# Optimization experiments

Hardware: AMD Instinct MI355X
Metric: run time of the kernel (lower is better)

Reference implementation:

```python
import jax, jax.numpy as jnp
import numpy as np

N_HEADS = 8
HIDDEN = 256
D_HEAD = HIDDEN // N_HEADS
N_NODES = 4096
N_EDGES = 16384


def setup_inputs() -> dict:
    key = jax.random.key(0)
    ks = jax.random.split(key, 12)
    s = 0.05
    return {
        "q": jax.random.normal(ks[0], (N_EDGES, HIDDEN), jnp.float32),
        "k": jax.random.normal(ks[1], (N_NODES, HIDDEN), jnp.float32),
        "v": jax.random.normal(ks[2], (N_NODES, HIDDEN), jnp.float32),
        "T": jax.random.uniform(ks[3], (N_NODES, N_EDGES), jnp.float32),
        "Wq": jax.random.normal(ks[4], (HIDDEN, HIDDEN), jnp.float32) * s,
        "bq": jax.random.normal(ks[5], (HIDDEN,), jnp.float32) * s,
        "Wk": jax.random.normal(ks[6], (HIDDEN, HIDDEN), jnp.float32) * s,
        "bk": jax.random.normal(ks[7], (HIDDEN,), jnp.float32) * s,
        "Wv": jax.random.normal(ks[8], (HIDDEN, HIDDEN), jnp.float32) * s,
        "bv": jax.random.normal(ks[9], (HIDDEN,), jnp.float32) * s,
        "Wo": jax.random.normal(ks[10], (HIDDEN, HIDDEN), jnp.float32) * s,
        "bo": jax.random.normal(ks[11], (HIDDEN,), jnp.float32) * s,
    }


def reference(q, k, v, T, Wq, bq, Wk, bk, Wv, bv, Wo, bo):
    scale = D_HEAD ** (-0.5)
    # projections, reshaped to per-head layout
    qh = (q @ Wq.T + bq).reshape(-1, N_HEADS, D_HEAD)  # [E, H, d]
    kh = (k @ Wk.T + bk).reshape(-1, N_HEADS, D_HEAD)  # [N, H, d]
    vh = (v @ Wv.T + bv).reshape(-1, N_HEADS, D_HEAD)  # [N, H, d]
    # row-normalized transition matrix (rows with zero sum left unscaled)
    row_sum = jnp.sum(T, axis=-1, keepdims=True)       # [N, 1]
    Tn = T / jnp.where(row_sum == 0, 1.0, row_sum)     # [N, E]
    # edge->node aggregation of queries, then scale
    qn = jnp.einsum("ne,ehd->nhd", Tn, qh) * scale     # [N, H, d]
    # attention: full NxN scores per head
    scores = jnp.einsum("nhd,mhd->hnm", qn, kh)        # [H, N, N]
    attn = jax.nn.softmax(scores, axis=-1)
    ctx = jnp.einsum("hnm,mhd->nhd", attn, vh)         # [N, H, d]
    out = ctx.reshape(-1, N_HEADS * D_HEAD) @ Wo.T + bo  # [N, hidden]
    return out
```

## Files before the change

### kernel.cpp

```cpp
#include <hip/hip_runtime.h>


#define N_NODES 4096
#define N_EDGES 16384
#define HIDDEN  256
#define KSPLIT  16

typedef __attribute__((ext_vector_type(4))) float f32x4;
typedef __attribute__((ext_vector_type(8))) short s16x8;
typedef __attribute__((ext_vector_type(4))) unsigned short u16x4;
typedef __attribute__((ext_vector_type(8))) unsigned short u16x8;

__device__ __forceinline__ unsigned short f2bf(float f) {
    union { float f; unsigned u; } x; x.f = f;
    unsigned r = x.u + 0x7FFFu + ((x.u >> 16) & 1u);
    return (unsigned short)(r >> 16);
}
__device__ __forceinline__ s16x8 pack8s(f32x4 x, f32x4 y) {
    u16x8 o;
    o[0]=f2bf(x[0]); o[1]=f2bf(x[1]); o[2]=f2bf(x[2]); o[3]=f2bf(x[3]);
    o[4]=f2bf(y[0]); o[5]=f2bf(y[1]); o[6]=f2bf(y[2]); o[7]=f2bf(y[3]);
    union { u16x8 u; s16x8 s; } c; c.u = o; return c.s;
}

__global__ __launch_bounds__(256)
void cvtW(const float* __restrict__ Wq, const float* __restrict__ Wk,
          const float* __restrict__ Wv, const float* __restrict__ Wo,
          unsigned short* __restrict__ dst)
{
    const int g = blockIdx.x * 256 + threadIdx.x;
    const long base = (long)g * 8;
    const int mat = (int)(base >> 16), off = (int)(base & 65535);
    const float* src = (mat == 0) ? Wq : (mat == 1) ? Wk : (mat == 2) ? Wv : Wo;
    f32x4 x = *(const f32x4*)&src[off];
    f32x4 y = *(const f32x4*)&src[off + 4];
    union { u16x8 u; s16x8 s; } c; c.s = pack8s(x, y);
    *(u16x8*)&dst[base] = c.u;
}

template<int MODE>
__global__ __launch_bounds__(256)
void proj_mfma(const float* __restrict__ A, const unsigned short* __restrict__ Wbf,
               const float* __restrict__ bias, unsigned short* __restrict__ out, int M)
{
    const int t = threadIdx.x;
    const int w = t >> 6, l = t & 63, lo = l & 15, h4 = l >> 4;
    const int m0 = blockIdx.x * 64 + w * 16;
    const int bn = blockIdx.y * 64;
    const float* Ar = A + (long)(m0 + lo) * 256 + h4 * 8;

    f32x4 acc[4] = {};
    #pragma unroll
    for (int kk = 0; kk < 8; ++kk) {
        f32x4 x = *(const f32x4*)&Ar[kk * 32];
        f32x4 y = *(const f32x4*)&Ar[kk * 32 + 4];
        s16x8 af = pack8s(x, y);
        #pragma unroll
        for (int nj = 0; nj < 4; ++nj) {
            s16x8 bf = *(const s16x8*)&Wbf[(bn + nj * 16 + lo) * 256 + kk * 32 + h4 * 8];
            acc[nj] = __builtin_amdgcn_mfma_f32_16x16x32_bf16(af, bf, acc[nj], 0, 0, 0);
        }
    }
    #pragma unroll
    for (int nj = 0; nj < 4; ++nj) {
        const int n = bn + nj * 16 + lo;
        const float bi = bias[n];
        if (MODE == 1) {
            #pragma unroll
            for (int r = 0; r < 4; ++r)
                out[(long)(m0 + h4 * 4 + r) * 256 + n] = f2bf(acc[nj][r] + bi);
        } else {
            u16x4 o;
            #pragma unroll
            for (int r = 0; r < 4; ++r) o[r] = f2bf(acc[nj][r] + bi);
            *(u16x4*)&out[(long)n * M + m0 + h4 * 4] = o;
        }
    }
}

__global__ __launch_bounds__(256)
void proj_out_mfma(const float* __restrict__ pctx, const float* __restrict__ plp,
                   const unsigned short* __restrict__ Wobf, const float* __restrict__ bo,
                   float* __restrict__ out)
{
    const int t = threadIdx.x;
    const int w = t >> 6, l = t & 63, lo = l & 15, h4 = l >> 4;
    const int m0 = blockIdx.x * 64 + w * 16;
    const int bn = blockIdx.y * 64;
    const int m = m0 + lo;

    float inv[8];
    #pragma unroll
    for (int h = 0; h < 8; ++h) {
        float s = plp[(0 * 8 + h) * N_NODES + m] + plp[(1 * 8 + h) * N_NODES + m]
                + plp[(2 * 8 + h) * N_NODES + m] + plp[(3 * 8 + h) * N_NODES + m];
        inv[h] = 1.0f / s;
    }
    const float* P = pctx + (long)m * 256;
    const long PS = (long)N_NODES * 256;

    f32x4 acc[4] = {};
    #pragma unroll
    for (int kk = 0; kk < 8; ++kk) {
        const int off = kk * 32 + h4 * 8;
        f32x4 x = *(const f32x4*)&P[off]          + *(const f32x4*)&P[PS + off]
                + *(const f32x4*)&P[2 * PS + off] + *(const f32x4*)&P[3 * PS + off];
        f32x4 y = *(const f32x4*)&P[off + 4]          + *(const f32x4*)&P[PS + off + 4]
                + *(const f32x4*)&P[2 * PS + off + 4] + *(const f32x4*)&P[3 * PS + off + 4];
        s16x8 af = pack8s(x * inv[kk], y * inv[kk]);
        #pragma unroll
        for (int nj = 0; nj < 4; ++nj) {
            s16x8 bf = *(const s16x8*)&Wobf[(bn + nj * 16 + lo) * 256 + kk * 32 + h4 * 8];
            acc[nj] = __builtin_amdgcn_mfma_f32_16x16x32_bf16(af, bf, acc[nj], 0, 0, 0);
        }
    }
    #pragma unroll
    for (int nj = 0; nj < 4; ++nj) {
        const int n = bn + nj * 16 + lo;
        const float bi = bo[n];
        #pragma unroll
        for (int r = 0; r < 4; ++r)
            out[(long)(m0 + h4 * 4 + r) * 256 + n] = acc[nj][r] + bi;
    }
}

__global__ __launch_bounds__(512, 4)
void tgemm(const float* __restrict__ T, const unsigned short* __restrict__ Bt,
           float* __restrict__ part, float* __restrict__ rsp)
{
    __shared__ __align__(16) unsigned short Bsm[2][256 * 64];
    const int t  = threadIdx.x;
    const int ks = blockIdx.x & 15, ms = blockIdx.x >> 4;
    const int m0 = ms * 128;
    const long k00 = (long)ks * 1024;
    const int w = t >> 6, l = t & 63, lo = l & 15, h4 = l >> 4;

    const int kx = ((l & 7) * 8) ^ ((l >> 3) << 3);
    const unsigned short* Bsrc = Bt + k00 + kx;

#define STAGE(itv, bufv) do {                                                       \
    const unsigned short* _s = Bsrc + (long)(itv) * 64;                             \
    unsigned short* _d = &Bsm[(bufv)][w * 2048];                                    \
    _Pragma("unroll")                                                               \
    for (int _i = 0; _i < 4; ++_i)                                                  \
        __builtin_amdgcn_global_load_lds(                                           \
            (const __attribute__((address_space(1))) unsigned int*)                 \
                (_s + (long)(w * 32 + _i * 8 + (l >> 3)) * N_EDGES),                \
            (__attribute__((address_space(3))) unsigned int*)(_d + _i * 512),       \
            16, 0, 0);                                                              \
} while (0)

    const float* Arow = T + (long)(m0 + w * 16 + lo) * N_EDGES + k00 + h4 * 8;

    STAGE(0, 0);
    f32x4 a0 = *(const f32x4*)&Arow[0];
    f32x4 a1 = *(const f32x4*)&Arow[4];
    f32x4 a2 = *(const f32x4*)&Arow[32];
    f32x4 a3 = *(const f32x4*)&Arow[36];
    __syncthreads();

    f32x4 acc[16] = {};
    float rs = 0.f;

    for (int it = 0; it < 16; ++it) {
        const int cur = it & 1;
        if (it < 15) STAGE(it + 1, cur ^ 1);
        s16x8 af0 = pack8s(a0, a1);
        s16x8 af1 = pack8s(a2, a3);
        rs += a0[0]+a0[1]+a0[2]+a0[3] + a1[0]+a1[1]+a1[2]+a1[3]
            + a2[0]+a2[1]+a2[2]+a2[3] + a3[0]+a3[1]+a3[2]+a3[3];
        if (it < 15) {
            const float* An = Arow + (it + 1) * 64;
            a0 = *(const f32x4*)&An[0];
            a1 = *(const f32x4*)&An[4];
            a2 = *(const f32x4*)&An[32];
            a3 = *(const f32x4*)&An[36];
        }
        const unsigned short* Bb = Bsm[cur];
        const int swz = (lo & 7) << 3;
        #pragma unroll
        for (int nj = 0; nj < 16; ++nj) {
            const int jb = (nj * 16 + lo) * 64;
            s16x8 bf0 = *(const s16x8*)&Bb[jb + ((h4 * 8) ^ swz)];
            s16x8 bf1 = *(const s16x8*)&Bb[jb + ((32 + h4 * 8) ^ swz)];
            acc[nj] = __builtin_amdgcn_mfma_f32_16x16x32_bf16(af0, bf0, acc[nj], 0, 0, 0);
            acc[nj] = __builtin_amdgcn_mfma_f32_16x16x32_bf16(af1, bf1, acc[nj], 0, 0, 0);
        }
        __syncthreads();
    }
#undef STAGE

    rs += __shfl_xor(rs, 16); rs += __shfl_xor(rs, 32);
    if (h4 == 0) rsp[ks * N_NODES + m0 + w * 16 + lo] = rs;

    float* P = part + (long)ks * (N_NODES * HIDDEN);
    #pragma unroll
    for (int nj = 0; nj < 16; ++nj)
        #pragma unroll
        for (int r = 0; r < 4; ++r)
            P[(long)(m0 + w * 16 + h4 * 4 + r) * HIDDEN + nj * 16 + lo] = acc[nj][r];
}

__global__ __launch_bounds__(256)
void finalize(const float* __restrict__ part, const float* __restrict__ rsp,
              unsigned short* __restrict__ qn)
{
    const int idx = blockIdx.x * 256 + threadIdx.x;
    const long i4 = (long)idx * 4;
    const int n = (int)(i4 >> 8);
    f32x4 s = {};
    #pragma unroll
    for (int ksp = 0; ksp < KSPLIT; ++ksp)
        s += *(const f32x4*)&part[(long)ksp * (N_NODES * HIDDEN) + i4];
    float rs = 0.f;
    #pragma unroll
    for (int ksp = 0; ksp < KSPLIT; ++ksp) rs += rsp[ksp * N_NODES + n];
    rs = (rs == 0.0f) ? 1.0f : rs;
    const float sc = 0.17677669529663687f / rs;
    u16x4 o;
    #pragma unroll
    for (int i = 0; i < 4; ++i) o[i] = f2bf(s[i] * sc);
    *(u16x4*)&qn[i4] = o;
}

__global__ __launch_bounds__(256)
void attn(const unsigned short* __restrict__ qn, const unsigned short* __restrict__ kh,
          const unsigned short* __restrict__ vht, float* __restrict__ pctx,
          float* __restrict__ plp)
{
    __shared__ __align__(16) unsigned short Ksm[64 * 40];
    __shared__ __align__(16) unsigned short Vsm[32 * 72];
    __shared__ __align__(16) unsigned short Psm[4][32 * 72];
    const int t  = threadIdx.x;
    const int hh = blockIdx.x >> 7, nb = (blockIdx.x >> 2) & 31, mh = blockIdx.x & 3;
    const int w = t >> 6, l = t & 63, lo = l & 15, h4 = l >> 4;
    const int n0 = nb * 128 + w * 32;

    const int km = t >> 2, kdc = (t & 3) * 8;
    const int vd = t >> 3, vmc = (t & 7) * 8;

    s16x8 qf[2];
    #pragma unroll
    for (int ni = 0; ni < 2; ++ni)
        qf[ni] = *(const s16x8*)&qn[(long)(n0 + ni * 16 + lo) * HIDDEN + hh * 32 + h4 * 8];

    f32x4 acc[2][2] = {};
    float lp[2][4] = {};
    const f32x4 zero = {};

    for (int mt = mh * 16; mt < mh * 16 + 16; ++mt) {
        const int m0 = mt * 64;
        *(s16x8*)&Ksm[km * 40 + kdc] =
            *(const s16x8*)&kh[(long)(m0 + km) * HIDDEN + hh * 32 + kdc];
        *(s16x8*)&Vsm[vd * 72 + vmc] =
            *(const s16x8*)&vht[(long)(hh * 32 + vd) * N_NODES + m0 + vmc];
        __syncthreads();

        s16x8 kb[4];
        #pragma unroll
        for (int mi = 0; mi < 4; ++mi)
            kb[mi] = *(const s16x8*)&Ksm[(mi * 16 + lo) * 40 + h4 * 8];
        #pragma unroll
        for (int ni = 0; ni < 2; ++ni) {
            #pragma unroll
            for (int mi = 0; mi < 4; ++mi) {
                f32x4 s = __builtin_amdgcn_mfma_f32_16x16x32_bf16(qf[ni], kb[mi], zero, 0, 0, 0);
                #pragma unroll
                for (int r = 0; r < 4; ++r) {
                    float p = __expf(s[r]);
                    lp[ni][r] += p;
                    Psm[w][(ni * 16 + h4 * 4 + r) * 72 + mi * 16 + lo] = f2bf(p);
                }
            }
        }
        s16x8 pa[2][2], vb[2][2];
        #pragma unroll
        for (int ni = 0; ni < 2; ++ni)
            #pragma unroll
            for (int k2 = 0; k2 < 2; ++k2)
                pa[ni][k2] = *(const s16x8*)&Psm[w][(ni * 16 + lo) * 72 + k2 * 32 + h4 * 8];
        #pragma unroll
        for (int di = 0; di < 2; ++di)
            #pragma unroll
            for (int k2 = 0; k2 < 2; ++k2)
                vb[di][k2] = *(const s16x8*)&Vsm[(di * 16 + lo) * 72 + k2 * 32 + h4 * 8];
        #pragma unroll
        for (int k2 = 0; k2 < 2; ++k2)
            #pragma unroll
            for (int ni = 0; ni < 2; ++ni)
                #pragma unroll
                for (int di = 0; di < 2; ++di)
                    acc[ni][di] = __builtin_amdgcn_mfma_f32_16x16x32_bf16(
                        pa[ni][k2], vb[di][k2], acc[ni][di], 0, 0, 0);
        __syncthreads();
    }
    #pragma unroll
    for (int ni = 0; ni < 2; ++ni)
        #pragma unroll
        for (int r = 0; r < 4; ++r) {
            float v2 = lp[ni][r];
            v2 += __shfl_xor(v2, 1); v2 += __shfl_xor(v2, 2);
            v2 += __shfl_xor(v2, 4); v2 += __shfl_xor(v2, 8);
            lp[ni][r] = v2;
        }
    float* myctx = pctx + (long)mh * (N_NODES * HIDDEN);
    float* myplp = plp  + (long)(mh * 8 + hh) * N_NODES;
    if (lo == 0)
        #pragma unroll
        for (int ni = 0; ni < 2; ++ni)
            #pragma unroll
            for (int r = 0; r < 4; ++r)
                myplp[n0 + ni * 16 + h4 * 4 + r] = lp[ni][r];
    #pragma unroll
    for (int ni = 0; ni < 2; ++ni)
        #pragma unroll
        for (int di = 0; di < 2; ++di)
            #pragma unroll
            for (int r = 0; r < 4; ++r)
                myctx[(long)(n0 + ni * 16 + h4 * 4 + r) * HIDDEN + hh * 32 + di * 16 + lo]
                    = acc[ni][di][r];
}

extern "C" void kernel_launch(void* const* d_in, const int* in_sizes, int n_in,
                              void* d_out, int out_size, void* d_ws, size_t ws_size,
                              hipStream_t stream)
{
    const float* q  = (const float*)d_in[0];
    const float* k  = (const float*)d_in[1];
    const float* v  = (const float*)d_in[2];
    const float* T  = (const float*)d_in[3];
    const float* Wq = (const float*)d_in[4];  const float* bq = (const float*)d_in[5];
    const float* Wk = (const float*)d_in[6];  const float* bk = (const float*)d_in[7];
    const float* Wv = (const float*)d_in[8];  const float* bv = (const float*)d_in[9];
    const float* Wo = (const float*)d_in[10]; const float* bo = (const float*)d_in[11];

    char* w = (char*)d_ws;
    unsigned short* qh_t = (unsigned short*)(w);
    unsigned short* kh   = (unsigned short*)(w + (8u  << 20));
    unsigned short* vh_t = (unsigned short*)(w + (10u << 20));
    unsigned short* qn   = (unsigned short*)(w + (12u << 20));
    float*          pctx = (float*)         (w + (14u << 20));
    float*          plp  = (float*)         (w + (30u << 20));
    float*          part = (float*)         (w + (32u << 20));
    float*          rsp  = (float*)         (w + (96u << 20));
    unsigned short* wbf  = (unsigned short*)(w + (97u << 20));
    unsigned short* wq_bf = wbf;
    unsigned short* wk_bf = wbf + 65536;
    unsigned short* wv_bf = wbf + 2 * 65536;
    unsigned short* wo_bf = wbf + 3 * 65536;

    cvtW<<<128, 256, 0, stream>>>(Wq, Wk, Wv, Wo, wbf);
    proj_mfma<2><<<dim3(256, 4), 256, 0, stream>>>(q, wq_bf, bq, qh_t, N_EDGES);
    proj_mfma<1><<<dim3(64, 4),  256, 0, stream>>>(k, wk_bf, bk, kh,   N_NODES);
    proj_mfma<2><<<dim3(64, 4),  256, 0, stream>>>(v, wv_bf, bv, vh_t, N_NODES);
    tgemm<<<512, 512, 0, stream>>>(T, qh_t, part, rsp);
    finalize<<<1024, 256, 0, stream>>>(part, rsp, qn);
    attn<<<1024, 256, 0, stream>>>(qn, kh, vh_t, pctx, plp);
    proj_out_mfma<<<dim3(64, 4), 256, 0, stream>>>(pctx, plp, wo_bf, bo, (float*)d_out);
}
```

Before: 214.7 us.

## Drop weight-conversion kernel, restructure projections, use nontemporal loads/stores

```diff
diff --git a/kernel.cpp b/kernel.cpp
--- a/kernel.cpp
+++ b/kernel.cpp
@@ -24,103 +24,148 @@
 }
 
 __global__ __launch_bounds__(256)
-void cvtW(const float* __restrict__ Wq, const float* __restrict__ Wk,
-          const float* __restrict__ Wv, const float* __restrict__ Wo,
-          unsigned short* __restrict__ dst)
-{
-    const int g = blockIdx.x * 256 + threadIdx.x;
-    const long base = (long)g * 8;
-    const int mat = (int)(base >> 16), off = (int)(base & 65535);
-    const float* src = (mat == 0) ? Wq : (mat == 1) ? Wk : (mat == 2) ? Wv : Wo;
-    f32x4 x = *(const f32x4*)&src[off];
-    f32x4 y = *(const f32x4*)&src[off + 4];
-    union { u16x8 u; s16x8 s; } c; c.s = pack8s(x, y);
-    *(u16x8*)&dst[base] = c.u;
-}
-
-template<int MODE>
+void proj_t(const float* __restrict__ A, const float* __restrict__ W,
+            const float* __restrict__ bias, unsigned short* __restrict__ out, int M)
+{
+    const int t = threadIdx.x;
+    const int w = t >> 6, l = t & 63, lo = l & 15, h4 = l >> 4;
+    const int m0 = blockIdx.x * 64;
+    const int n0 = w * 64;
+
+    f32x4 bv[4];
+    #pragma unroll
+    for (int nj = 0; nj < 4; ++nj) bv[nj] = *(const f32x4*)&bias[n0 + nj * 16 + h4 * 4];
+
+    f32x4 acc[4][4] = {};
+    #pragma unroll
+    for (int kk = 0; kk < 8; ++kk) {
+        const int ko = kk * 32 + h4 * 8;
+        s16x8 bq[4];
+        #pragma unroll
+        for (int mi = 0; mi < 4; ++mi) {
+            f32x4 x = *(const f32x4*)&A[(long)(m0 + mi * 16 + lo) * 256 + ko];
+            f32x4 y = *(const f32x4*)&A[(long)(m0 + mi * 16 + lo) * 256 + ko + 4];
+            bq[mi] = pack8s(x, y);
+        }
+        #pragma unroll
+        for (int nj = 0; nj < 4; ++nj) {
+            f32x4 wx = *(const f32x4*)&W[(n0 + nj * 16 + lo) * 256 + ko];
+            f32x4 wy = *(const f32x4*)&W[(n0 + nj * 16 + lo) * 256 + ko + 4];
+            s16x8 af = pack8s(wx, wy);
+            #pragma unroll
+            for (int mi = 0; mi < 4; ++mi)
+                acc[nj][mi] = __builtin_amdgcn_mfma_f32_16x16x32_bf16(af, bq[mi], acc[nj][mi], 0, 0, 0);
+        }
+    }
+    #pragma unroll
+    for (int nj = 0; nj < 4; ++nj)
+        #pragma unroll
+        for (int r = 0; r < 4; ++r) {
+            const long nrow = (long)(n0 + nj * 16 + h4 * 4 + r) * M;
+            const float bi = bv[nj][r];
+            #pragma unroll
+            for (int mi = 0; mi < 4; ++mi)
+                out[nrow + m0 + mi * 16 + lo] = f2bf(acc[nj][mi][r] + bi);
+        }
+}
+
 __global__ __launch_bounds__(256)
-void proj_mfma(const float* __restrict__ A, const unsigned short* __restrict__ Wbf,
-               const float* __restrict__ bias, unsigned short* __restrict__ out, int M)
+void proj_r(const float* __restrict__ A, const float* __restrict__ W,
+            const float* __restrict__ bias, unsigned short* __restrict__ out)
 {
     const int t = threadIdx.x;
     const int w = t >> 6, l = t & 63, lo = l & 15, h4 = l >> 4;
     const int m0 = blockIdx.x * 64 + w * 16;
-    const int bn = blockIdx.y * 64;
-    const float* Ar = A + (long)(m0 + lo) * 256 + h4 * 8;
-
-    f32x4 acc[4] = {};
+
+    s16x8 af[8];
     #pragma unroll
     for (int kk = 0; kk < 8; ++kk) {
-        f32x4 x = *(const f32x4*)&Ar[kk * 32];
-        f32x4 y = *(const f32x4*)&Ar[kk * 32 + 4];
-        s16x8 af = pack8s(x, y);
+        const int ko = kk * 32 + h4 * 8;
+        f32x4 x = *(const f32x4*)&A[(long)(m0 + lo) * 256 + ko];
+        f32x4 y = *(const f32x4*)&A[(long)(m0 + lo) * 256 + ko + 4];
+        af[kk] = pack8s(x, y);
+    }
+    #pragma unroll
+    for (int bn = 0; bn < 4; ++bn) {
+        f32x4 acc[4] = {};
+        #pragma unroll
+        for (int kk = 0; kk < 8; ++kk) {
+            const int ko = kk * 32 + h4 * 8;
+            #pragma unroll
+            for (int nj = 0; nj < 4; ++nj) {
+                const int n = bn * 64 + nj * 16 + lo;
+                f32x4 wx = *(const f32x4*)&W[n * 256 + ko];
+                f32x4 wy = *(const f32x4*)&W[n * 256 + ko + 4];
+                acc[nj] = __builtin_amdgcn_mfma_f32_16x16x32_bf16(af[kk], pack8s(wx, wy), acc[nj], 0, 0, 0);
+            }
+        }
         #pragma unroll
         for (int nj = 0; nj < 4; ++nj) {
-            s16x8 bf = *(const s16x8*)&Wbf[(bn + nj * 16 + lo) * 256 + kk * 32 + h4 * 8];
-            acc[nj] = __builtin_amdgcn_mfma_f32_16x16x32_bf16(af, bf, acc[nj], 0, 0, 0);
-        }
-    }
-    #pragma unroll
-    for (int nj = 0; nj < 4; ++nj) {
-        const int n = bn + nj * 16 + lo;
-        const float bi = bias[n];
-        if (MODE == 1) {
+            const int n = bn * 64 + nj * 16 + lo;
+            const float bi = bias[n];
             #pragma unroll
             for (int r = 0; r < 4; ++r)
                 out[(long)(m0 + h4 * 4 + r) * 256 + n] = f2bf(acc[nj][r] + bi);
-        } else {
-            u16x4 o;
-            #pragma unroll
-            for (int r = 0; r < 4; ++r) o[r] = f2bf(acc[nj][r] + bi);
-            *(u16x4*)&out[(long)n * M + m0 + h4 * 4] = o;
         }
     }
 }
 
 __global__ __launch_bounds__(256)
 void proj_out_mfma(const float* __restrict__ pctx, const float* __restrict__ plp,
-                   const unsigned short* __restrict__ Wobf, const float* __restrict__ bo,
+                   const float* __restrict__ W, const float* __restrict__ bo,
                    float* __restrict__ out)
 {
     const int t = threadIdx.x;
     const int w = t >> 6, l = t & 63, lo = l & 15, h4 = l >> 4;
     const int m0 = blockIdx.x * 64 + w * 16;
-    const int bn = blockIdx.y * 64;
     const int m = m0 + lo;
 
     float inv[8];
     #pragma unroll
     for (int h = 0; h < 8; ++h) {
-        float s = plp[(0 * 8 + h) * N_NODES + m] + plp[(1 * 8 + h) * N_NODES + m]
-                + plp[(2 * 8 + h) * N_NODES + m] + plp[(3 * 8 + h) * N_NODES + m];
+        float s = plp[h * N_NODES + m]        + plp[(8 + h) * N_NODES + m]
+                + plp[(16 + h) * N_NODES + m] + plp[(24 + h) * N_NODES + m];
         inv[h] = 1.0f / s;
     }
     const float* P = pctx + (long)m * 256;
     const long PS = (long)N_NODES * 256;
 
-    f32x4 acc[4] = {};
+    s16x8 af[8];
     #pragma unroll
     for (int kk = 0; kk < 8; ++kk) {
         const int off = kk * 32 + h4 * 8;
-        f32x4 x = *(const f32x4*)&P[off]          + *(const f32x4*)&P[PS + off]
-                + *(const f32x4*)&P[2 * PS + off] + *(const f32x4*)&P[3 * PS + off];
-        f32x4 y = *(const f32x4*)&P[off + 4]          + *(const f32x4*)&P[PS + off + 4]
-                + *(const f32x4*)&P[2 * PS + off + 4] + *(const f32x4*)&P[3 * PS + off + 4];
-        s16x8 af = pack8s(x * inv[kk], y * inv[kk]);
+        f32x4 x = __builtin_nontemporal_load((const f32x4*)&P[off])
+                + __builtin_nontemporal_load((const f32x4*)&P[PS + off])
+                + __builtin_nontemporal_load((const f32x4*)&P[2 * PS + off])
+                + __builtin_nontemporal_load((const f32x4*)&P[3 * PS + off]);
+        f32x4 y = __builtin_nontemporal_load((const f32x4*)&P[off + 4])
+                + __builtin_nontemporal_load((const f32x4*)&P[PS + off + 4])
+                + __builtin_nontemporal_load((const f32x4*)&P[2 * PS + off + 4])
+                + __builtin_nontemporal_load((const f32x4*)&P[3 * PS + off + 4]);
+        af[kk] = pack8s(x * inv[kk], y * inv[kk]);
+    }
+    #pragma unroll
+    for (int bn = 0; bn < 4; ++bn) {
+        f32x4 acc[4] = {};
+        #pragma unroll
+        for (int kk = 0; kk < 8; ++kk) {
+            const int ko = kk * 32 + h4 * 8;
+            #pragma unroll
+            for (int nj = 0; nj < 4; ++nj) {
+                const int n = bn * 64 + nj * 16 + lo;
+                f32x4 wx = *(const f32x4*)&W[n * 256 + ko];
+                f32x4 wy = *(const f32x4*)&W[n * 256 + ko + 4];
+                acc[nj] = __builtin_amdgcn_mfma_f32_16x16x32_bf16(af[kk], pack8s(wx, wy), acc[nj], 0, 0, 0);
+            }
+        }
         #pragma unroll
         for (int nj = 0; nj < 4; ++nj) {
-            s16x8 bf = *(const s16x8*)&Wobf[(bn + nj * 16 + lo) * 256 + kk * 32 + h4 * 8];
-            acc[nj] = __builtin_amdgcn_mfma_f32_16x16x32_bf16(af, bf, acc[nj], 0, 0, 0);
-        }
-    }
-    #pragma unroll
-    for (int nj = 0; nj < 4; ++nj) {
-        const int n = bn + nj * 16 + lo;
-        const float bi = bo[n];
-        #pragma unroll
-        for (int r = 0; r < 4; ++r)
-            out[(long)(m0 + h4 * 4 + r) * 256 + n] = acc[nj][r] + bi;
+            const int n = bn * 64 + nj * 16 + lo;
+            const float bi = bo[n];
+            #pragma unroll
+            for (int r = 0; r < 4; ++r)
+                out[(long)(m0 + h4 * 4 + r) * 256 + n] = acc[nj][r] + bi;
+        }
     }
 }
 
@@ -153,10 +198,10 @@
     const float* Arow = T + (long)(m0 + w * 16 + lo) * N_EDGES + k00 + h4 * 8;
 
     STAGE(0, 0);
-    f32x4 a0 = *(const f32x4*)&Arow[0];
-    f32x4 a1 = *(const f32x4*)&Arow[4];
-    f32x4 a2 = *(const f32x4*)&Arow[32];
-    f32x4 a3 = *(const f32x4*)&Arow[36];
+    f32x4 a0 = __builtin_nontemporal_load((const f32x4*)&Arow[0]);
+    f32x4 a1 = __builtin_nontemporal_load((const f32x4*)&Arow[4]);
+    f32x4 a2 = __builtin_nontemporal_load((const f32x4*)&Arow[32]);
+    f32x4 a3 = __builtin_nontemporal_load((const f32x4*)&Arow[36]);
     __syncthreads();
 
     f32x4 acc[16] = {};
@@ -171,10 +216,10 @@
             + a2[0]+a2[1]+a2[2]+a2[3] + a3[0]+a3[1]+a3[2]+a3[3];
         if (it < 15) {
             const float* An = Arow + (it + 1) * 64;
-            a0 = *(const f32x4*)&An[0];
-            a1 = *(const f32x4*)&An[4];
-            a2 = *(const f32x4*)&An[32];
-            a3 = *(const f32x4*)&An[36];
+            a0 = __builtin_nontemporal_load((const f32x4*)&An[0]);
+            a1 = __builtin_nontemporal_load((const f32x4*)&An[4]);
+            a2 = __builtin_nontemporal_load((const f32x4*)&An[32]);
+            a3 = __builtin_nontemporal_load((const f32x4*)&An[36]);
         }
         const unsigned short* Bb = Bsm[cur];
         const int swz = (lo & 7) << 3;
@@ -198,7 +243,8 @@
     for (int nj = 0; nj < 16; ++nj)
         #pragma unroll
         for (int r = 0; r < 4; ++r)
-            P[(long)(m0 + w * 16 + h4 * 4 + r) * HIDDEN + nj * 16 + lo] = acc[nj][r];
+            __builtin_nontemporal_store(acc[nj][r],
+                &P[(long)(m0 + w * 16 + h4 * 4 + r) * HIDDEN + nj * 16 + lo]);
 }
 
 __global__ __launch_bounds__(256)
@@ -211,7 +257,7 @@
     f32x4 s = {};
     #pragma unroll
     for (int ksp = 0; ksp < KSPLIT; ++ksp)
-        s += *(const f32x4*)&part[(long)ksp * (N_NODES * HIDDEN) + i4];
+        s += __builtin_nontemporal_load((const f32x4*)&part[(long)ksp * (N_NODES * HIDDEN) + i4]);
     float rs = 0.f;
     #pragma unroll
     for (int ksp = 0; ksp < KSPLIT; ++ksp) rs += rsp[ksp * N_NODES + n];
@@ -317,8 +363,8 @@
         for (int di = 0; di < 2; ++di)
             #pragma unroll
             for (int r = 0; r < 4; ++r)
-                myctx[(long)(n0 + ni * 16 + h4 * 4 + r) * HIDDEN + hh * 32 + di * 16 + lo]
-                    = acc[ni][di][r];
+                __builtin_nontemporal_store(acc[ni][di][r],
+                    &myctx[(long)(n0 + ni * 16 + h4 * 4 + r) * HIDDEN + hh * 32 + di * 16 + lo]);
 }
 
 extern "C" void kernel_launch(void* const* d_in, const int* in_sizes, int n_in,
@@ -343,18 +389,12 @@
     float*          plp  = (float*)         (w + (30u << 20));
     float*          part = (float*)         (w + (32u << 20));
     float*          rsp  = (float*)         (w + (96u << 20));
-    unsigned short* wbf  = (unsigned short*)(w + (97u << 20));
-    unsigned short* wq_bf = wbf;
-    unsigned short* wk_bf = wbf + 65536;
-    unsigned short* wv_bf = wbf + 2 * 65536;
-    unsigned short* wo_bf = wbf + 3 * 65536;
-
-    cvtW<<<128, 256, 0, stream>>>(Wq, Wk, Wv, Wo, wbf);
-    proj_mfma<2><<<dim3(256, 4), 256, 0, stream>>>(q, wq_bf, bq, qh_t, N_EDGES);
-    proj_mfma<1><<<dim3(64, 4),  256, 0, stream>>>(k, wk_bf, bk, kh,   N_NODES);
-    proj_mfma<2><<<dim3(64, 4),  256, 0, stream>>>(v, wv_bf, bv, vh_t, N_NODES);
+
+    proj_t<<<256, 256, 0, stream>>>(q, Wq, bq, qh_t, N_EDGES);
+    proj_r<<<64,  256, 0, stream>>>(k, Wk, bk, kh);
+    proj_t<<<64,  256, 0, stream>>>(v, Wv, bv, vh_t, N_NODES);
     tgemm<<<512, 512, 0, stream>>>(T, qh_t, part, rsp);
     finalize<<<1024, 256, 0, stream>>>(part, rsp, qn);
     attn<<<1024, 256, 0, stream>>>(qn, kh, vh_t, pctx, plp);
-    proj_out_mfma<<<dim3(64, 4), 256, 0, stream>>>(pctx, plp, wo_bf, bo, (float*)d_out);
-}
+    proj_out_mfma<<<64, 256, 0, stream>>>(pctx, plp, Wo, bo, (float*)d_out);
+}
```

New measurement: 340.4 us. 58.5% more time.
